# Kernel tuning notes

Measured on AMD Instinct MI355X. Metric: run time of the kernel, lower is better.

The kernel has to match this reference:

```python
import jax, jax.numpy as jnp
import numpy as np

D_MODEL = 1024
NUM_HEADS = 16
NUM_KV_HEADS = 4
D_K = D_MODEL // NUM_HEADS              # 64
G = NUM_HEADS // NUM_KV_HEADS           # queries per kv head = 4
B, S = 2, 2048


def setup_inputs() -> dict:
    key = jax.random.key(0)
    ks = jax.random.split(key, 11)
    s = 0.02
    return {
        "query": jax.random.normal(ks[0], (B, S, D_MODEL), jnp.float32),
        "key_in": jax.random.normal(ks[1], (B, S, D_MODEL), jnp.float32),
        "value_in": jax.random.normal(ks[2], (B, S, D_MODEL), jnp.float32),
        "Wq": jax.random.normal(ks[3], (D_MODEL, D_MODEL), jnp.float32) * s,
        "bq": jnp.zeros((D_MODEL,), jnp.float32),
        "Wk": jax.random.normal(ks[4], (D_MODEL, NUM_KV_HEADS * D_K), jnp.float32) * s,
        "bk": jnp.zeros((NUM_KV_HEADS * D_K,), jnp.float32),
        "Wv": jax.random.normal(ks[5], (D_MODEL, NUM_KV_HEADS * D_K), jnp.float32) * s,
        "bv": jnp.zeros((NUM_KV_HEADS * D_K,), jnp.float32),
        "Wo": jax.random.normal(ks[6], (D_MODEL, D_MODEL), jnp.float32) * s,
        "bo": jnp.zeros((D_MODEL,), jnp.float32),
    }


def reference(query, key_in, value_in, Wq, bq, Wk, bk, Wv, bv, Wo, bo):
    scale = jnp.sqrt(jnp.asarray(D_K, query.dtype))
    # Projections
    Q = (query @ Wq + bq).reshape(B, S, NUM_HEADS, D_K).transpose(0, 2, 1, 3)        # [B,H,S,dk]
    K = (key_in @ Wk + bk).reshape(B, S, NUM_KV_HEADS, D_K).transpose(0, 2, 1, 3)    # [B,KVH,S,dk]
    V = (value_in @ Wv + bv).reshape(B, S, NUM_KV_HEADS, D_K).transpose(0, 2, 1, 3)  # [B,KVH,S,dk]
    # repeat_interleave over head dim -> group Q heads by KV head instead
    Qg = Q.reshape(B, NUM_KV_HEADS, G, S, D_K)                                       # [B,KVH,G,S,dk]
    scores = jnp.einsum('bkgqd,bksd->bkgqs', Qg, K) / scale                          # [B,KVH,G,S,S]
    attn = jax.nn.softmax(scores, axis=-1)
    ctx = jnp.einsum('bkgqs,bksd->bkgqd', attn, V)                                   # [B,KVH,G,S,dk]
    ctx = ctx.reshape(B, NUM_HEADS, S, D_K).transpose(0, 2, 1, 3).reshape(B, S, D_MODEL)
    output = ctx @ Wo + bo
    # new_cache: K[:, ::G] on the repeated tensor == original K/V per kv head
    return output, K, V
```

## Files before the change

kernel.cpp:

```cpp
#include <hip/hip_runtime.h>

typedef unsigned short u16;
typedef unsigned int u32;
typedef __attribute__((ext_vector_type(8))) short short8;
typedef __attribute__((ext_vector_type(4))) float f32x4;

#define MFMA16(a, b, c) __builtin_amdgcn_mfma_f32_16x16x32_bf16(a, b, c, 0, 0, 0)

#define SEQ 2048
#define DM 1024

__device__ __forceinline__ u32 pack2(float a, float b) {
  u32 r;
  asm("v_cvt_pk_bf16_f32 %0, %1, %2" : "=v"(r) : "v"(a), "v"(b));
  return r;
}
__device__ __forceinline__ u32 pack2t(float a, float b) {
  return __builtin_amdgcn_perm(__float_as_uint(b), __float_as_uint(a), 0x07060302u);
}
__device__ __forceinline__ void pswap32(u32& a, u32& b) {
  asm("v_permlane32_swap_b32 %0, %1" : "+v"(a), "+v"(b));
}
__device__ __forceinline__ void pswap16(u32& a, u32& b) {
  asm("v_permlane16_swap_b32 %0, %1" : "+v"(a), "+v"(b));
}
__device__ __forceinline__ void gload16(const u16* g, u16* l) {
  __builtin_amdgcn_global_load_lds((const __attribute__((address_space(1))) u32*)g,
                                   (__attribute__((address_space(3))) u32*)l, 16, 0, 0);
}

#define MBF 0
#define MF32 1
#define MTR 2

template <int AM, int BM>
__device__ __forceinline__ void gemm64(const void* __restrict__ A, const void* __restrict__ B,
                                       int m0, int n0, int ldA, int ldB, u16* lA, u16* lB,
                                       f32x4 acc[2][4]) {
  const int tid = threadIdx.x;
  const int lane = tid & 63, wave = tid >> 6;
  const int l15 = lane & 15, quad = lane >> 4;
  const int wm = wave >> 1, wn = wave & 1;
  const int sr = tid >> 3, sch = tid & 7;
  const int gr = lane >> 3, gch = (lane & 7) ^ (lane >> 3);
  const int nb = tid & 127, ko = tid >> 7;
  f32x4 zero = {0.f, 0.f, 0.f, 0.f};
#pragma unroll
  for (int i = 0; i < 2; i++)
#pragma unroll
    for (int j = 0; j < 4; j++) acc[i][j] = zero;

  float rA[16], rB[32];

  auto issue = [&](int k0, u16* dA, u16* dB) {
    if constexpr (AM == MBF) {
#pragma unroll
      for (int it = 0; it < 2; it++) {
        int w8 = wave * 2 + it;
        gload16((const u16*)A + (size_t)(m0 + w8 * 8 + gr) * ldA + k0 + gch * 8,
                dA + w8 * 512);
      }
    } else if constexpr (AM == MF32) {
#pragma unroll
      for (int it = 0; it < 2; it++) {
        const float* p = (const float*)A + (size_t)(m0 + sr + it * 32) * ldA + k0 + sch * 8;
        float4 a = *(const float4*)p, b = *(const float4*)(p + 4);
        rA[it * 8 + 0] = a.x; rA[it * 8 + 1] = a.y; rA[it * 8 + 2] = a.z; rA[it * 8 + 3] = a.w;
        rA[it * 8 + 4] = b.x; rA[it * 8 + 5] = b.y; rA[it * 8 + 6] = b.z; rA[it * 8 + 7] = b.w;
      }
    } else {
      const float* Wf = (const float*)A;
#pragma unroll
      for (int j = 0; j < 16; j++)
        rA[j] = Wf[(size_t)(k0 + wave * 16 + j) * ldA + m0 + lane];
    }
    if constexpr (BM == MBF) {
#pragma unroll
      for (int it = 0; it < 4; it++) {
        int w8 = wave * 4 + it;
        gload16((const u16*)B + (size_t)(n0 + w8 * 8 + gr) * ldB + k0 + gch * 8,
                dB + w8 * 512);
      }
    } else if constexpr (BM == MF32) {
#pragma unroll
      for (int it = 0; it < 4; it++) {
        const float* p = (const float*)B + (size_t)(n0 + sr + it * 32) * ldB + k0 + sch * 8;
        float4 a = *(const float4*)p, b = *(const float4*)(p + 4);
        rB[it * 8 + 0] = a.x; rB[it * 8 + 1] = a.y; rB[it * 8 + 2] = a.z; rB[it * 8 + 3] = a.w;
        rB[it * 8 + 4] = b.x; rB[it * 8 + 5] = b.y; rB[it * 8 + 6] = b.z; rB[it * 8 + 7] = b.w;
      }
    } else {
      const float* Wf = (const float*)B;
#pragma unroll
      for (int j = 0; j < 32; j++)
        rB[j] = Wf[(size_t)(k0 + ko * 32 + j) * ldB + n0 + nb];
    }
  };

  auto wrb = [&](u16* dA, u16* dB) {
    if constexpr (AM == MF32) {
#pragma unroll
      for (int it = 0; it < 2; it++) {
        int r = sr + it * 32;
        uint4 v;
        v.x = pack2(rA[it * 8 + 0], rA[it * 8 + 1]);
        v.y = pack2(rA[it * 8 + 2], rA[it * 8 + 3]);
        v.z = pack2(rA[it * 8 + 4], rA[it * 8 + 5]);
        v.w = pack2(rA[it * 8 + 6], rA[it * 8 + 7]);
        *(uint4*)&dA[r * 64 + ((sch ^ (r & 7)) << 3)] = v;
      }
    } else if constexpr (AM == MTR) {
#pragma unroll
      for (int o = 0; o < 2; o++) {
        uint4 v;
        v.x = pack2(rA[o * 8 + 0], rA[o * 8 + 1]);
        v.y = pack2(rA[o * 8 + 2], rA[o * 8 + 3]);
        v.z = pack2(rA[o * 8 + 4], rA[o * 8 + 5]);
        v.w = pack2(rA[o * 8 + 6], rA[o * 8 + 7]);
        int c = (wave * 2 + o) ^ (lane & 7);
        *(uint4*)&dA[lane * 64 + (c << 3)] = v;
      }
    }
    if constexpr (BM == MF32) {
#pragma unroll
      for (int it = 0; it < 4; it++) {
        int r = sr + it * 32;
        uint4 v;
        v.x = pack2(rB[it * 8 + 0], rB[it * 8 + 1]);
        v.y = pack2(rB[it * 8 + 2], rB[it * 8 + 3]);
        v.z = pack2(rB[it * 8 + 4], rB[it * 8 + 5]);
        v.w = pack2(rB[it * 8 + 6], rB[it * 8 + 7]);
        *(uint4*)&dB[r * 64 + ((sch ^ (r & 7)) << 3)] = v;
      }
    } else if constexpr (BM == MTR) {
#pragma unroll
      for (int o = 0; o < 4; o++) {
        uint4 v;
        v.x = pack2(rB[o * 8 + 0], rB[o * 8 + 1]);
        v.y = pack2(rB[o * 8 + 2], rB[o * 8 + 3]);
        v.z = pack2(rB[o * 8 + 4], rB[o * 8 + 5]);
        v.w = pack2(rB[o * 8 + 6], rB[o * 8 + 7]);
        int c = (ko * 4 + o) ^ (nb & 7);
        *(uint4*)&dB[nb * 64 + (c << 3)] = v;
      }
    }
  };

  issue(0, lA, lB);
  wrb(lA, lB);
  __syncthreads();

  for (int t = 0; t < 16; t++) {
    u16* cA = lA + (t & 1) * 4096;
    u16* cB = lB + (t & 1) * 8192;
    u16* nA = lA + ((t + 1) & 1) * 4096;
    u16* nB = lB + ((t + 1) & 1) * 8192;
    if (t < 15) issue((t + 1) * 64, nA, nB);
    short8 af[2][2], bfr[4][2];
#pragma unroll
    for (int i = 0; i < 2; i++)
#pragma unroll
      for (int kb = 0; kb < 2; kb++) {
        int r = wm * 32 + i * 16 + l15;
        af[i][kb] = *(const short8*)&cA[r * 64 + (((kb * 4 + quad) ^ (r & 7)) << 3)];
      }
#pragma unroll
    for (int j = 0; j < 4; j++)
#pragma unroll
      for (int kb = 0; kb < 2; kb++) {
        int r = wn * 64 + j * 16 + l15;
        bfr[j][kb] = *(const short8*)&cB[r * 64 + (((kb * 4 + quad) ^ (r & 7)) << 3)];
      }
#pragma unroll
    for (int i = 0; i < 2; i++)
#pragma unroll
      for (int j = 0; j < 4; j++) {
        acc[i][j] = MFMA16(af[i][0], bfr[j][0], acc[i][j]);
        acc[i][j] = MFMA16(af[i][1], bfr[j][1], acc[i][j]);
      }
    if (t < 15) wrb(nA, nB);
    __syncthreads();
  }
}

__global__ __launch_bounds__(256, 3) void k_proj(
    const float* __restrict__ query, const float* __restrict__ key_in,
    const float* __restrict__ value_in, const float* __restrict__ Wq,
    const float* __restrict__ Wk, const float* __restrict__ Wv, const float* __restrict__ bq,
    const float* __restrict__ bk, const float* __restrict__ bv, u16* __restrict__ qbf,
    float* __restrict__ outK, u16* __restrict__ kbf, float* __restrict__ outV,
    u16* __restrict__ vtb, float qscale) {
  __shared__ u16 lA[2 * 4096];
  __shared__ u16 lB[2 * 8192];
  const int idx = blockIdx.x;
  const int lane = threadIdx.x & 63, wave = threadIdx.x >> 6;
  const int l15 = lane & 15, quad = lane >> 4;
  const int wm = wave >> 1, wn = wave & 1;
  f32x4 acc[2][4];

  if (idx < 640) {
    const float* Wt;
    const float* act;
    const float* bias;
    int m0, n0, ldW, mode;
    if (idx < 512) {
      Wt = Wq; act = query; bias = bq; ldW = 1024;
      m0 = (idx >> 5) * 64; n0 = (idx & 31) * 128; mode = 0;
    } else {
      int i2 = idx - 512;
      Wt = Wk; act = key_in; bias = bk; ldW = 256;
      m0 = (i2 >> 5) * 64; n0 = (i2 & 31) * 128; mode = 1;
    }
    gemm64<MTR, MF32>(Wt, act, m0, n0, ldW, 1024, lA, lB, acc);
#pragma unroll
    for (int i = 0; i < 2; i++) {
      int c0 = m0 + wm * 32 + i * 16 + quad * 4;
      float4 bb = *(const float4*)(bias + c0);
#pragma unroll
      for (int j = 0; j < 4; j++) {
        int token = n0 + wn * 64 + j * 16 + l15;
        int b = token >> 11, s = token & 2047;
        float v0 = acc[i][j][0] + bb.x, v1 = acc[i][j][1] + bb.y;
        float v2 = acc[i][j][2] + bb.z, v3 = acc[i][j][3] + bb.w;
        int d = c0 & 63;
        if (mode == 0) {
          int h = c0 >> 6;
          uint2 o;
          o.x = pack2(v0 * qscale, v1 * qscale);
          o.y = pack2(v2 * qscale, v3 * qscale);
          *(uint2*)(qbf + (((size_t)(b * 16 + h) * SEQ + s) << 6) + d) = o;
        } else {
          int kvh = c0 >> 6;
          size_t ix = (((size_t)(b * 4 + kvh) * SEQ + s) << 6) + d;
          float4 vv = {v0, v1, v2, v3};
          *(float4*)(outK + ix) = vv;
          uint2 o;
          o.x = pack2(v0, v1);
          o.y = pack2(v2, v3);
          *(uint2*)(kbf + ix) = o;
        }
      }
    }
  } else {
    int i2 = idx - 640;
    int m0 = (i2 >> 1) * 64, n0 = (i2 & 1) * 128;
    gemm64<MF32, MTR>(value_in, Wv, m0, n0, 1024, 256, lA, lB, acc);
#pragma unroll
    for (int i = 0; i < 2; i++) {
      int r0 = m0 + wm * 32 + i * 16 + quad * 4;
      int b = r0 >> 11, s0 = r0 & 2047;
#pragma unroll
      for (int j = 0; j < 4; j++) {
        int col = n0 + wn * 64 + j * 16 + l15;
        int kvh = col >> 6, d = col & 63;
        float bv_ = bv[col];
        float v0 = acc[i][j][0] + bv_, v1 = acc[i][j][1] + bv_;
        float v2 = acc[i][j][2] + bv_, v3 = acc[i][j][3] + bv_;
        size_t base = (((size_t)(b * 4 + kvh) * SEQ + s0) << 6) + d;
        outV[base] = v0;
        outV[base + 64] = v1;
        outV[base + 128] = v2;
        outV[base + 192] = v3;
        uint2 o;
        o.x = pack2(v0, v1);
        o.y = pack2(v2, v3);
        *(uint2*)(vtb + ((size_t)(b * 4 + kvh) * 64 + d) * SEQ + s0) = o;
      }
    }
  }
}

__global__ __launch_bounds__(256, 2) void k_out(const u16* __restrict__ ctxb,
                                                const float* __restrict__ Wo,
                                                const float* __restrict__ bo,
                                                float* __restrict__ out) {
  __shared__ u16 lA[2 * 4096];
  __shared__ u16 lB[2 * 8192];
  const int idx = blockIdx.x;
  const int m0 = (idx >> 5) * 64, n0 = (idx & 31) * 128;
  const int lane = threadIdx.x & 63, wave = threadIdx.x >> 6;
  const int l15 = lane & 15, quad = lane >> 4;
  const int wm = wave >> 1, wn = wave & 1;
  f32x4 acc[2][4];
  gemm64<MTR, MBF>(Wo, ctxb, m0, n0, 1024, 1024, lA, lB, acc);
#pragma unroll
  for (int i = 0; i < 2; i++) {
    int c0 = m0 + wm * 32 + i * 16 + quad * 4;
    float4 bb = *(const float4*)(bo + c0);
#pragma unroll
    for (int j = 0; j < 4; j++) {
      int token = n0 + wn * 64 + j * 16 + l15;
      float4 vv = {acc[i][j][0] + bb.x, acc[i][j][1] + bb.y, acc[i][j][2] + bb.z,
                   acc[i][j][3] + bb.w};
      *(float4*)(out + (size_t)token * DM + c0) = vv;
    }
  }
}

__global__ __launch_bounds__(256, 2) void k_flash(const u16* __restrict__ Qh,
                                                  const u16* __restrict__ Kb,
                                                  const u16* __restrict__ Vt,
                                                  u16* __restrict__ ctx) {
  __shared__ u16 lK[2][128 * 64];
  __shared__ u16 lV[2][64 * 128];
  const int tid = threadIdx.x;
  const int lane = tid & 63, wave = tid >> 6;
  const int l15 = lane & 15, quad = lane >> 4;
  const int bh = blockIdx.y;
  const int b = bh >> 4, h = bh & 15, kvh = h >> 2;
  const u16* Q = Qh + (size_t)bh * SEQ * 64;
  const u16* Kp = Kb + (size_t)(b * 4 + kvh) * SEQ * 64;
  const u16* Vp = Vt + (size_t)(b * 4 + kvh) * 64 * SEQ;
  const int q0 = blockIdx.x * 128 + wave * 32;

  short8 qf[2][2];
#pragma unroll
  for (int g = 0; g < 2; g++)
#pragma unroll
    for (int kb = 0; kb < 2; kb++)
      qf[g][kb] = *(const short8*)(Q + (size_t)(q0 + g * 16 + l15) * 64 + kb * 32 + quad * 8);

  short8 ones8;
  {
    short ov = (l15 == 0) ? (short)0x3F80 : (short)0;
    ones8 = (short8){ov, ov, ov, ov, ov, ov, ov, ov};
  }

  f32x4 zero = {0.f, 0.f, 0.f, 0.f};
  f32x4 acc[2][4];
  f32x4 lacc[2] = {zero, zero};
#pragma unroll
  for (int g = 0; g < 2; g++)
#pragma unroll
    for (int n = 0; n < 4; n++) acc[g][n] = zero;

  const int gr3 = lane >> 3, gc7 = lane & 7;
  const int gr4 = lane >> 4, gc15 = lane & 15;

  auto stage = [&](int kc, int bufi) {
    u16* dK = lK[bufi];
    u16* dV = lV[bufi];
#pragma unroll
    for (int i = 0; i < 4; i++) {
      int slab = wave * 4 + i;
      gload16(Kp + (size_t)(kc + slab * 8 + gr3) * 64 + ((gc7 ^ gr3) << 3), dK + slab * 512);
    }
#pragma unroll
    for (int i = 0; i < 4; i++) {
      int slab = wave * 4 + i;
      int row = slab * 4 + gr4;
      gload16(Vp + (size_t)row * SEQ + kc + ((gc15 ^ (row & 15)) << 3), dV + slab * 512);
    }
  };

  stage(0, 0);
  __syncthreads();

  for (int t = 0; t < SEQ / 128; t++) {
    if (t < SEQ / 128 - 1) stage((t + 1) * 128, (t + 1) & 1);
    const u16* cK = lK[t & 1];
    const u16* cV = lV[t & 1];

#pragma unroll
    for (int sub = 0; sub < 2; sub++) {
      const int ks = sub * 64;
      f32x4 sc[2][4];
#pragma unroll
      for (int mt = 0; mt < 4; mt++) {
        int row = ks + mt * 16 + l15;
        short8 kf0 = *(const short8*)&cK[row * 64 + ((quad ^ (row & 7)) << 3)];
        short8 kf1 = *(const short8*)&cK[row * 64 + (((4 + quad) ^ (row & 7)) << 3)];
#pragma unroll
        for (int g = 0; g < 2; g++) {
          f32x4 t0 = MFMA16(kf0, qf[g][0], zero);
          sc[g][mt] = MFMA16(kf1, qf[g][1], t0);
        }
      }
#pragma unroll
      for (int g = 0; g < 2; g++)
#pragma unroll
        for (int mt = 0; mt < 4; mt++)
#pragma unroll
          for (int r = 0; r < 4; r++) sc[g][mt][r] = __builtin_amdgcn_exp2f(sc[g][mt][r]);

#pragma unroll
      for (int kbp = 0; kbp < 2; kbp++) {
        short8 pf[2];
#pragma unroll
        for (int g = 0; g < 2; g++) {
          u32 U0 = pack2t(sc[g][2 * kbp][0], sc[g][2 * kbp][1]);
          u32 W0 = pack2t(sc[g][2 * kbp + 1][0], sc[g][2 * kbp + 1][1]);
          u32 U1 = pack2t(sc[g][2 * kbp][2], sc[g][2 * kbp][3]);
          u32 W1 = pack2t(sc[g][2 * kbp + 1][2], sc[g][2 * kbp + 1][3]);
          pswap32(U0, W0);
          pswap16(U0, W0);
          pswap32(U1, W1);
          pswap16(U1, W1);
          u32 w[4] = {U0, U1, W0, W1};
          pf[g] = *(const short8*)w;
        }
        lacc[0] = MFMA16(ones8, pf[0], lacc[0]);
        lacc[1] = MFMA16(ones8, pf[1], lacc[1]);
#pragma unroll
        for (int n = 0; n < 4; n++) {
          int row = n * 16 + l15;
          int chv = sub * 8 + kbp * 4 + quad;
          short8 vf = *(const short8*)&cV[row * 128 + ((chv ^ (row & 15)) << 3)];
          acc[0][n] = MFMA16(vf, pf[0], acc[0][n]);
          acc[1][n] = MFMA16(vf, pf[1], acc[1][n]);
        }
      }
    }
    __syncthreads();
  }

#pragma unroll
  for (int g = 0; g < 2; g++) {
    float lq = __shfl(lacc[g][0], l15);
    float inv = __builtin_amdgcn_rcpf(lq);
    u16* base = ctx + ((size_t)(b * SEQ + q0 + g * 16 + l15)) * DM + h * 64;
#pragma unroll
    for (int n = 0; n < 4; n++) {
      uint2 o;
      o.x = pack2t(acc[g][n][0] * inv, acc[g][n][1] * inv);
      o.y = pack2t(acc[g][n][2] * inv, acc[g][n][3] * inv);
      *(uint2*)(base + n * 16 + quad * 4) = o;
    }
  }
}

extern "C" void kernel_launch(void* const* d_in, const int* in_sizes, int n_in,
                              void* d_out, int out_size, void* d_ws, size_t ws_size,
                              hipStream_t stream) {
  const float* query = (const float*)d_in[0];
  const float* key_in = (const float*)d_in[1];
  const float* value_in = (const float*)d_in[2];
  const float* Wq = (const float*)d_in[3];
  const float* bq = (const float*)d_in[4];
  const float* Wk = (const float*)d_in[5];
  const float* bk = (const float*)d_in[6];
  const float* Wv = (const float*)d_in[7];
  const float* bv = (const float*)d_in[8];
  const float* Wo = (const float*)d_in[9];
  const float* bo = (const float*)d_in[10];

  float* out = (float*)d_out;
  float* outK = out + 4194304;
  float* outV = out + 5242880;

  char* ws = (char*)d_ws;
  u16* qbf = (u16*)(ws + 5242880);
  u16* kbf = (u16*)(ws + 13631488);
  u16* vtb = (u16*)(ws + 15728640);
  u16* ctxb = (u16*)(ws + 17825792);

  const float qscale = 0.125f * 1.44269504088896340736f;

  k_proj<<<dim3(768), 256, 0, stream>>>(query, key_in, value_in, Wq, Wk, Wv, bq, bk, bv,
                                        qbf, outK, kbf, outV, vtb, qscale);
  k_flash<<<dim3(16, 32), 256, 0, stream>>>(qbf, kbf, vtb, ctxb);
  k_out<<<dim3(512), 256, 0, stream>>>(ctxb, Wo, bo, out);
}
```

Measured before the change: 218.0 us.

## Pre-transpose weights and query to bf16 in a prep kernel for async LDS loads

New measurement: 201.3 us. -7.7%, faster.

```diff
diff --git a/kernel.cpp b/kernel.cpp
--- a/kernel.cpp
+++ b/kernel.cpp
@@ -10,6 +10,11 @@
 #define SEQ 2048
 #define DM 1024
 
+__device__ __forceinline__ u16 f2bf(float f) {
+  u32 u = __float_as_uint(f);
+  u += 0x7fffu + ((u >> 16) & 1u);
+  return (u16)(u >> 16);
+}
 __device__ __forceinline__ u32 pack2(float a, float b) {
   u32 r;
   asm("v_cvt_pk_bf16_f32 %0, %1, %2" : "=v"(r) : "v"(a), "v"(b));
@@ -29,9 +34,50 @@
                                    (__attribute__((address_space(3))) u32*)l, 16, 0, 0);
 }
 
+__global__ __launch_bounds__(256) void k_prep(const float* __restrict__ Wq,
+                                              const float* __restrict__ Wk,
+                                              const float* __restrict__ Wv,
+                                              const float* __restrict__ Wo,
+                                              const float* __restrict__ query,
+                                              u16* __restrict__ WqT, u16* __restrict__ WkT,
+                                              u16* __restrict__ WvT, u16* __restrict__ WoT,
+                                              u16* __restrict__ qact) {
+  const int blk = blockIdx.x;
+  const int tid = threadIdx.x;
+  if (blk >= 4096) {
+    size_t base = (size_t)(blk - 4096) * 4096 + tid * 16;
+    const float* p = query + base;
+    uint4 o0, o1;
+    float4 a = *(const float4*)p, b = *(const float4*)(p + 4);
+    float4 c = *(const float4*)(p + 8), d = *(const float4*)(p + 12);
+    o0.x = pack2(a.x, a.y); o0.y = pack2(a.z, a.w);
+    o0.z = pack2(b.x, b.y); o0.w = pack2(b.z, b.w);
+    o1.x = pack2(c.x, c.y); o1.y = pack2(c.z, c.w);
+    o1.z = pack2(d.x, d.y); o1.w = pack2(d.z, d.w);
+    *(uint4*)(qact + base) = o0;
+    *(uint4*)(qact + base + 8) = o1;
+    return;
+  }
+  const int z = blk >> 10, r = blk & 1023;
+  const float* W = z == 0 ? Wq : (z == 1 ? Wk : (z == 2 ? Wv : Wo));
+  u16* Wt = z == 0 ? WqT : (z == 1 ? WkT : (z == 2 ? WvT : WoT));
+  const int N = (z == 1 || z == 2) ? 256 : 1024;
+  const int n0 = (r & 31) * 32;
+  if (n0 >= N) return;
+  const int k0 = (r >> 5) * 32;
+  __shared__ float tile[32][33];
+  int x = tid & 31, y = tid >> 5;
+#pragma unroll
+  for (int i = 0; i < 4; i++)
+    tile[y + i * 8][x] = W[(size_t)(k0 + y + i * 8) * N + n0 + x];
+  __syncthreads();
+#pragma unroll
+  for (int i = 0; i < 4; i++)
+    Wt[(size_t)(n0 + y + i * 8) * 1024 + k0 + x] = f2bf(tile[x][y + i * 8]);
+}
+
 #define MBF 0
 #define MF32 1
-#define MTR 2
 
 template <int AM, int BM>
 __device__ __forceinline__ void gemm64(const void* __restrict__ A, const void* __restrict__ B,
@@ -43,7 +89,6 @@
   const int wm = wave >> 1, wn = wave & 1;
   const int sr = tid >> 3, sch = tid & 7;
   const int gr = lane >> 3, gch = (lane & 7) ^ (lane >> 3);
-  const int nb = tid & 127, ko = tid >> 7;
   f32x4 zero = {0.f, 0.f, 0.f, 0.f};
 #pragma unroll
   for (int i = 0; i < 2; i++)
@@ -60,7 +105,7 @@
         gload16((const u16*)A + (size_t)(m0 + w8 * 8 + gr) * ldA + k0 + gch * 8,
                 dA + w8 * 512);
       }
-    } else if constexpr (AM == MF32) {
+    } else {
 #pragma unroll
       for (int it = 0; it < 2; it++) {
         const float* p = (const float*)A + (size_t)(m0 + sr + it * 32) * ldA + k0 + sch * 8;
@@ -68,11 +113,6 @@
         rA[it * 8 + 0] = a.x; rA[it * 8 + 1] = a.y; rA[it * 8 + 2] = a.z; rA[it * 8 + 3] = a.w;
         rA[it * 8 + 4] = b.x; rA[it * 8 + 5] = b.y; rA[it * 8 + 6] = b.z; rA[it * 8 + 7] = b.w;
       }
-    } else {
-      const float* Wf = (const float*)A;
-#pragma unroll
-      for (int j = 0; j < 16; j++)
-        rA[j] = Wf[(size_t)(k0 + wave * 16 + j) * ldA + m0 + lane];
     }
     if constexpr (BM == MBF) {
 #pragma unroll
@@ -81,7 +121,7 @@
         gload16((const u16*)B + (size_t)(n0 + w8 * 8 + gr) * ldB + k0 + gch * 8,
                 dB + w8 * 512);
       }
-    } else if constexpr (BM == MF32) {
+    } else {
 #pragma unroll
       for (int it = 0; it < 4; it++) {
         const float* p = (const float*)B + (size_t)(n0 + sr + it * 32) * ldB + k0 + sch * 8;
@@ -89,11 +129,6 @@
         rB[it * 8 + 0] = a.x; rB[it * 8 + 1] = a.y; rB[it * 8 + 2] = a.z; rB[it * 8 + 3] = a.w;
         rB[it * 8 + 4] = b.x; rB[it * 8 + 5] = b.y; rB[it * 8 + 6] = b.z; rB[it * 8 + 7] = b.w;
       }
-    } else {
-      const float* Wf = (const float*)B;
-#pragma unroll
-      for (int j = 0; j < 32; j++)
-        rB[j] = Wf[(size_t)(k0 + ko * 32 + j) * ldB + n0 + nb];
     }
   };
 
@@ -109,17 +144,6 @@
         v.w = pack2(rA[it * 8 + 6], rA[it * 8 + 7]);
         *(uint4*)&dA[r * 64 + ((sch ^ (r & 7)) << 3)] = v;
       }
-    } else if constexpr (AM == MTR) {
-#pragma unroll
-      for (int o = 0; o < 2; o++) {
-        uint4 v;
-        v.x = pack2(rA[o * 8 + 0], rA[o * 8 + 1]);
-        v.y = pack2(rA[o * 8 + 2], rA[o * 8 + 3]);
-        v.z = pack2(rA[o * 8 + 4], rA[o * 8 + 5]);
-        v.w = pack2(rA[o * 8 + 6], rA[o * 8 + 7]);
-        int c = (wave * 2 + o) ^ (lane & 7);
-        *(uint4*)&dA[lane * 64 + (c << 3)] = v;
-      }
     }
     if constexpr (BM == MF32) {
 #pragma unroll
@@ -132,17 +156,6 @@
         v.w = pack2(rB[it * 8 + 6], rB[it * 8 + 7]);
         *(uint4*)&dB[r * 64 + ((sch ^ (r & 7)) << 3)] = v;
       }
-    } else if constexpr (BM == MTR) {
-#pragma unroll
-      for (int o = 0; o < 4; o++) {
-        uint4 v;
-        v.x = pack2(rB[o * 8 + 0], rB[o * 8 + 1]);
-        v.y = pack2(rB[o * 8 + 2], rB[o * 8 + 3]);
-        v.z = pack2(rB[o * 8 + 4], rB[o * 8 + 5]);
-        v.w = pack2(rB[o * 8 + 6], rB[o * 8 + 7]);
-        int c = (ko * 4 + o) ^ (nb & 7);
-        *(uint4*)&dB[nb * 64 + (c << 3)] = v;
-      }
     }
   };
 
@@ -184,9 +197,9 @@
 }
 
 __global__ __launch_bounds__(256, 3) void k_proj(
-    const float* __restrict__ query, const float* __restrict__ key_in,
-    const float* __restrict__ value_in, const float* __restrict__ Wq,
-    const float* __restrict__ Wk, const float* __restrict__ Wv, const float* __restrict__ bq,
+    const u16* __restrict__ qact, const float* __restrict__ key_in,
+    const float* __restrict__ value_in, const u16* __restrict__ WqT,
+    const u16* __restrict__ WkT, const u16* __restrict__ WvT, const float* __restrict__ bq,
     const float* __restrict__ bk, const float* __restrict__ bv, u16* __restrict__ qbf,
     float* __restrict__ outK, u16* __restrict__ kbf, float* __restrict__ outV,
     u16* __restrict__ vtb, float qscale) {
@@ -198,53 +211,54 @@
   const int wm = wave >> 1, wn = wave & 1;
   f32x4 acc[2][4];
 
-  if (idx < 640) {
-    const float* Wt;
-    const float* act;
-    const float* bias;
-    int m0, n0, ldW, mode;
-    if (idx < 512) {
-      Wt = Wq; act = query; bias = bq; ldW = 1024;
-      m0 = (idx >> 5) * 64; n0 = (idx & 31) * 128; mode = 0;
-    } else {
-      int i2 = idx - 512;
-      Wt = Wk; act = key_in; bias = bk; ldW = 256;
-      m0 = (i2 >> 5) * 64; n0 = (i2 & 31) * 128; mode = 1;
-    }
-    gemm64<MTR, MF32>(Wt, act, m0, n0, ldW, 1024, lA, lB, acc);
+  if (idx < 512) {
+    int m0 = (idx >> 5) * 64, n0 = (idx & 31) * 128;
+    gemm64<MBF, MBF>(WqT, qact, m0, n0, 1024, 1024, lA, lB, acc);
 #pragma unroll
     for (int i = 0; i < 2; i++) {
       int c0 = m0 + wm * 32 + i * 16 + quad * 4;
-      float4 bb = *(const float4*)(bias + c0);
+      float4 bb = *(const float4*)(bq + c0);
 #pragma unroll
       for (int j = 0; j < 4; j++) {
         int token = n0 + wn * 64 + j * 16 + l15;
         int b = token >> 11, s = token & 2047;
         float v0 = acc[i][j][0] + bb.x, v1 = acc[i][j][1] + bb.y;
         float v2 = acc[i][j][2] + bb.z, v3 = acc[i][j][3] + bb.w;
-        int d = c0 & 63;
-        if (mode == 0) {
-          int h = c0 >> 6;
-          uint2 o;
-          o.x = pack2(v0 * qscale, v1 * qscale);
-          o.y = pack2(v2 * qscale, v3 * qscale);
-          *(uint2*)(qbf + (((size_t)(b * 16 + h) * SEQ + s) << 6) + d) = o;
-        } else {
-          int kvh = c0 >> 6;
-          size_t ix = (((size_t)(b * 4 + kvh) * SEQ + s) << 6) + d;
-          float4 vv = {v0, v1, v2, v3};
-          *(float4*)(outK + ix) = vv;
-          uint2 o;
-          o.x = pack2(v0, v1);
-          o.y = pack2(v2, v3);
-          *(uint2*)(kbf + ix) = o;
-        }
+        int d = c0 & 63, h = c0 >> 6;
+        uint2 o;
+        o.x = pack2(v0 * qscale, v1 * qscale);
+        o.y = pack2(v2 * qscale, v3 * qscale);
+        *(uint2*)(qbf + (((size_t)(b * 16 + h) * SEQ + s) << 6) + d) = o;
+      }
+    }
+  } else if (idx < 640) {
+    int i2 = idx - 512;
+    int m0 = (i2 >> 5) * 64, n0 = (i2 & 31) * 128;
+    gemm64<MBF, MF32>(WkT, key_in, m0, n0, 1024, 1024, lA, lB, acc);
+#pragma unroll
+    for (int i = 0; i < 2; i++) {
+      int c0 = m0 + wm * 32 + i * 16 + quad * 4;
+      float4 bb = *(const float4*)(bk + c0);
+#pragma unroll
+      for (int j = 0; j < 4; j++) {
+        int token = n0 + wn * 64 + j * 16 + l15;
+        int b = token >> 11, s = token & 2047;
+        float v0 = acc[i][j][0] + bb.x, v1 = acc[i][j][1] + bb.y;
+        float v2 = acc[i][j][2] + bb.z, v3 = acc[i][j][3] + bb.w;
+        int d = c0 & 63, kvh = c0 >> 6;
+        size_t ix = (((size_t)(b * 4 + kvh) * SEQ + s) << 6) + d;
+        float4 vv = {v0, v1, v2, v3};
+        *(float4*)(outK + ix) = vv;
+        uint2 o;
+        o.x = pack2(v0, v1);
+        o.y = pack2(v2, v3);
+        *(uint2*)(kbf + ix) = o;
       }
     }
   } else {
     int i2 = idx - 640;
     int m0 = (i2 >> 1) * 64, n0 = (i2 & 1) * 128;
-    gemm64<MF32, MTR>(value_in, Wv, m0, n0, 1024, 256, lA, lB, acc);
+    gemm64<MF32, MBF>(value_in, WvT, m0, n0, 1024, 1024, lA, lB, acc);
 #pragma unroll
     for (int i = 0; i < 2; i++) {
       int r0 = m0 + wm * 32 + i * 16 + quad * 4;
@@ -270,8 +284,8 @@
   }
 }
 
-__global__ __launch_bounds__(256, 2) void k_out(const u16* __restrict__ ctxb,
-                                                const float* __restrict__ Wo,
+__global__ __launch_bounds__(256, 3) void k_out(const u16* __restrict__ ctxb,
+                                                const u16* __restrict__ WoT,
                                                 const float* __restrict__ bo,
                                                 float* __restrict__ out) {
   __shared__ u16 lA[2 * 4096];
@@ -282,7 +296,7 @@
   const int l15 = lane & 15, quad = lane >> 4;
   const int wm = wave >> 1, wn = wave & 1;
   f32x4 acc[2][4];
-  gemm64<MTR, MBF>(Wo, ctxb, m0, n0, 1024, 1024, lA, lB, acc);
+  gemm64<MBF, MBF>(WoT, ctxb, m0, n0, 1024, 1024, lA, lB, acc);
 #pragma unroll
   for (int i = 0; i < 2; i++) {
     int c0 = m0 + wm * 32 + i * 16 + quad * 4;
@@ -449,15 +463,21 @@
   float* outV = out + 5242880;
 
   char* ws = (char*)d_ws;
-  u16* qbf = (u16*)(ws + 5242880);
-  u16* kbf = (u16*)(ws + 13631488);
-  u16* vtb = (u16*)(ws + 15728640);
-  u16* ctxb = (u16*)(ws + 17825792);
+  u16* WqT = (u16*)(ws);
+  u16* WkT = (u16*)(ws + 2097152);
+  u16* WvT = (u16*)(ws + 2621440);
+  u16* WoT = (u16*)(ws + 3145728);
+  u16* qact = (u16*)(ws + 5242880);
+  u16* ctxb = (u16*)(ws + 5242880);
+  u16* qbf = (u16*)(ws + 13631488);
+  u16* kbf = (u16*)(ws + 22020096);
+  u16* vtb = (u16*)(ws + 24117248);
 
   const float qscale = 0.125f * 1.44269504088896340736f;
 
-  k_proj<<<dim3(768), 256, 0, stream>>>(query, key_in, value_in, Wq, Wk, Wv, bq, bk, bv,
+  k_prep<<<dim3(5120), 256, 0, stream>>>(Wq, Wk, Wv, Wo, query, WqT, WkT, WvT, WoT, qact);
+  k_proj<<<dim3(768), 256, 0, stream>>>(qact, key_in, value_in, WqT, WkT, WvT, bq, bk, bv,
                                         qbf, outK, kbf, outV, vtb, qscale);
   k_flash<<<dim3(16, 32), 256, 0, stream>>>(qbf, kbf, vtb, ctxb);
-  k_out<<<dim3(512), 256, 0, stream>>>(ctxb, Wo, bo, out);
-}
+  k_out<<<dim3(512), 256, 0, stream>>>(ctxb, WoT, bo, out);
+}
```

## Fuse Q projection into flash kernel and pre-convert weights to bf16

Applied to the files above, without the earlier changes.

Measured after the change: 208.1 us. 4.6% less time.

```diff
diff --git a/kernel.cpp b/kernel.cpp
--- a/kernel.cpp
+++ b/kernel.cpp
@@ -10,6 +10,11 @@
 #define SEQ 2048
 #define DM 1024
 
+__device__ __forceinline__ u16 f2bf(float f) {
+  u32 u = __float_as_uint(f);
+  u += 0x7fffu + ((u >> 16) & 1u);
+  return (u16)(u >> 16);
+}
 __device__ __forceinline__ u32 pack2(float a, float b) {
   u32 r;
   asm("v_cvt_pk_bf16_f32 %0, %1, %2" : "=v"(r) : "v"(a), "v"(b));
@@ -183,124 +188,110 @@
   }
 }
 
-__global__ __launch_bounds__(256, 3) void k_proj(
-    const float* __restrict__ query, const float* __restrict__ key_in,
-    const float* __restrict__ value_in, const float* __restrict__ Wq,
-    const float* __restrict__ Wk, const float* __restrict__ Wv, const float* __restrict__ bq,
-    const float* __restrict__ bk, const float* __restrict__ bv, u16* __restrict__ qbf,
-    float* __restrict__ outK, u16* __restrict__ kbf, float* __restrict__ outV,
-    u16* __restrict__ vtb, float qscale) {
-  __shared__ u16 lA[2 * 4096];
-  __shared__ u16 lB[2 * 8192];
+__global__ __launch_bounds__(256, 3) void k_pre(
+    const float* __restrict__ Wq, const float* __restrict__ Wk, const float* __restrict__ Wv,
+    const float* __restrict__ Wo, const float* __restrict__ query,
+    const float* __restrict__ key_in, const float* __restrict__ value_in,
+    const float* __restrict__ bk, const float* __restrict__ bv, u16* __restrict__ WqT,
+    u16* __restrict__ WoT, u16* __restrict__ qact, float* __restrict__ outK,
+    u16* __restrict__ kbf, float* __restrict__ outV, u16* __restrict__ vtb) {
+  __shared__ u16 lsd[2 * 4096 + 2 * 8192];
   const int idx = blockIdx.x;
-  const int lane = threadIdx.x & 63, wave = threadIdx.x >> 6;
-  const int l15 = lane & 15, quad = lane >> 4;
-  const int wm = wave >> 1, wn = wave & 1;
-  f32x4 acc[2][4];
-
-  if (idx < 640) {
-    const float* Wt;
-    const float* act;
-    const float* bias;
-    int m0, n0, ldW, mode;
-    if (idx < 512) {
-      Wt = Wq; act = query; bias = bq; ldW = 1024;
-      m0 = (idx >> 5) * 64; n0 = (idx & 31) * 128; mode = 0;
-    } else {
-      int i2 = idx - 512;
-      Wt = Wk; act = key_in; bias = bk; ldW = 256;
-      m0 = (i2 >> 5) * 64; n0 = (i2 & 31) * 128; mode = 1;
-    }
-    gemm64<MTR, MF32>(Wt, act, m0, n0, ldW, 1024, lA, lB, acc);
-#pragma unroll
-    for (int i = 0; i < 2; i++) {
-      int c0 = m0 + wm * 32 + i * 16 + quad * 4;
-      float4 bb = *(const float4*)(bias + c0);
-#pragma unroll
-      for (int j = 0; j < 4; j++) {
-        int token = n0 + wn * 64 + j * 16 + l15;
-        int b = token >> 11, s = token & 2047;
-        float v0 = acc[i][j][0] + bb.x, v1 = acc[i][j][1] + bb.y;
-        float v2 = acc[i][j][2] + bb.z, v3 = acc[i][j][3] + bb.w;
-        int d = c0 & 63;
-        if (mode == 0) {
-          int h = c0 >> 6;
-          uint2 o;
-          o.x = pack2(v0 * qscale, v1 * qscale);
-          o.y = pack2(v2 * qscale, v3 * qscale);
-          *(uint2*)(qbf + (((size_t)(b * 16 + h) * SEQ + s) << 6) + d) = o;
-        } else {
-          int kvh = c0 >> 6;
+  const int tid = threadIdx.x;
+
+  if (idx < 256) {
+    u16* lA = lsd;
+    u16* lB = lsd + 2 * 4096;
+    const int lane = tid & 63, wave = tid >> 6;
+    const int l15 = lane & 15, quad = lane >> 4;
+    const int wm = wave >> 1, wn = wave & 1;
+    f32x4 acc[2][4];
+    if (idx < 128) {
+      int m0 = (idx >> 5) * 64, n0 = (idx & 31) * 128;
+      gemm64<MTR, MF32>(Wk, key_in, m0, n0, 256, 1024, lA, lB, acc);
+#pragma unroll
+      for (int i = 0; i < 2; i++) {
+        int c0 = m0 + wm * 32 + i * 16 + quad * 4;
+        float4 bb = *(const float4*)(bk + c0);
+#pragma unroll
+        for (int j = 0; j < 4; j++) {
+          int token = n0 + wn * 64 + j * 16 + l15;
+          int b = token >> 11, s = token & 2047;
+          float v0 = acc[i][j][0] + bb.x, v1 = acc[i][j][1] + bb.y;
+          float v2 = acc[i][j][2] + bb.z, v3 = acc[i][j][3] + bb.w;
+          int d = c0 & 63, kvh = c0 >> 6;
           size_t ix = (((size_t)(b * 4 + kvh) * SEQ + s) << 6) + d;
           float4 vv = {v0, v1, v2, v3};
           *(float4*)(outK + ix) = vv;
-          uint2 o;
-          o.x = pack2(v0, v1);
-          o.y = pack2(v2, v3);
-          *(uint2*)(kbf + ix) = o;
+          uint2 ob;
+          ob.x = pack2(v0, v1);
+          ob.y = pack2(v2, v3);
+          *(uint2*)(kbf + ix) = ob;
         }
       }
-    }
+    } else {
+      int vi = idx - 128;
+      int m0 = (vi >> 1) * 64, n0 = (vi & 1) * 128;
+      gemm64<MF32, MTR>(value_in, Wv, m0, n0, 1024, 256, lA, lB, acc);
+#pragma unroll
+      for (int i = 0; i < 2; i++) {
+        int r0 = m0 + wm * 32 + i * 16 + quad * 4;
+        int b = r0 >> 11, s0 = r0 & 2047;
+#pragma unroll
+        for (int j = 0; j < 4; j++) {
+          int col = n0 + wn * 64 + j * 16 + l15;
+          int kvh = col >> 6, d = col & 63;
+          float bv_ = bv[col];
+          float v0 = acc[i][j][0] + bv_, v1 = acc[i][j][1] + bv_;
+          float v2 = acc[i][j][2] + bv_, v3 = acc[i][j][3] + bv_;
+          size_t base = (((size_t)(b * 4 + kvh) * SEQ + s0) << 6) + d;
+          outV[base] = v0;
+          outV[base + 64] = v1;
+          outV[base + 128] = v2;
+          outV[base + 192] = v3;
+          uint2 ob;
+          ob.x = pack2(v0, v1);
+          ob.y = pack2(v2, v3);
+          *(uint2*)(vtb + ((size_t)(b * 4 + kvh) * 64 + d) * SEQ + s0) = ob;
+        }
+      }
+    }
+  } else if (idx < 2304) {
+    float(*tile)[33] = (float(*)[33])lsd;
+    int wi = idx - 256;
+    const float* W = wi < 1024 ? Wq : Wo;
+    u16* Wt = wi < 1024 ? WqT : WoT;
+    wi &= 1023;
+    const int n0 = (wi & 31) * 32, k0 = (wi >> 5) * 32;
+    int x = tid & 31, y = tid >> 5;
+#pragma unroll
+    for (int i = 0; i < 4; i++)
+      tile[y + i * 8][x] = W[(size_t)(k0 + y + i * 8) * 1024 + n0 + x];
+    __syncthreads();
+#pragma unroll
+    for (int i = 0; i < 4; i++)
+      Wt[(size_t)(n0 + y + i * 8) * 1024 + k0 + x] = f2bf(tile[x][y + i * 8]);
   } else {
-    int i2 = idx - 640;
-    int m0 = (i2 >> 1) * 64, n0 = (i2 & 1) * 128;
-    gemm64<MF32, MTR>(value_in, Wv, m0, n0, 1024, 256, lA, lB, acc);
-#pragma unroll
-    for (int i = 0; i < 2; i++) {
-      int r0 = m0 + wm * 32 + i * 16 + quad * 4;
-      int b = r0 >> 11, s0 = r0 & 2047;
-#pragma unroll
-      for (int j = 0; j < 4; j++) {
-        int col = n0 + wn * 64 + j * 16 + l15;
-        int kvh = col >> 6, d = col & 63;
-        float bv_ = bv[col];
-        float v0 = acc[i][j][0] + bv_, v1 = acc[i][j][1] + bv_;
-        float v2 = acc[i][j][2] + bv_, v3 = acc[i][j][3] + bv_;
-        size_t base = (((size_t)(b * 4 + kvh) * SEQ + s0) << 6) + d;
-        outV[base] = v0;
-        outV[base + 64] = v1;
-        outV[base + 128] = v2;
-        outV[base + 192] = v3;
-        uint2 o;
-        o.x = pack2(v0, v1);
-        o.y = pack2(v2, v3);
-        *(uint2*)(vtb + ((size_t)(b * 4 + kvh) * 64 + d) * SEQ + s0) = o;
-      }
-    }
-  }
-}
-
-__global__ __launch_bounds__(256, 2) void k_out(const u16* __restrict__ ctxb,
-                                                const float* __restrict__ Wo,
-                                                const float* __restrict__ bo,
-                                                float* __restrict__ out) {
-  __shared__ u16 lA[2 * 4096];
-  __shared__ u16 lB[2 * 8192];
-  const int idx = blockIdx.x;
-  const int m0 = (idx >> 5) * 64, n0 = (idx & 31) * 128;
-  const int lane = threadIdx.x & 63, wave = threadIdx.x >> 6;
-  const int l15 = lane & 15, quad = lane >> 4;
-  const int wm = wave >> 1, wn = wave & 1;
-  f32x4 acc[2][4];
-  gemm64<MTR, MBF>(Wo, ctxb, m0, n0, 1024, 1024, lA, lB, acc);
-#pragma unroll
-  for (int i = 0; i < 2; i++) {
-    int c0 = m0 + wm * 32 + i * 16 + quad * 4;
-    float4 bb = *(const float4*)(bo + c0);
-#pragma unroll
-    for (int j = 0; j < 4; j++) {
-      int token = n0 + wn * 64 + j * 16 + l15;
-      float4 vv = {acc[i][j][0] + bb.x, acc[i][j][1] + bb.y, acc[i][j][2] + bb.z,
-                   acc[i][j][3] + bb.w};
-      *(float4*)(out + (size_t)token * DM + c0) = vv;
-    }
-  }
-}
-
-__global__ __launch_bounds__(256, 2) void k_flash(const u16* __restrict__ Qh,
+    size_t base = (size_t)(idx - 2304) * 4096 + tid * 16;
+    const float* p = query + base;
+    uint4 o0, o1;
+    float4 a = *(const float4*)p, b = *(const float4*)(p + 4);
+    float4 c = *(const float4*)(p + 8), d = *(const float4*)(p + 12);
+    o0.x = pack2(a.x, a.y); o0.y = pack2(a.z, a.w);
+    o0.z = pack2(b.x, b.y); o0.w = pack2(b.z, b.w);
+    o1.x = pack2(c.x, c.y); o1.y = pack2(c.z, c.w);
+    o1.z = pack2(d.x, d.y); o1.w = pack2(d.z, d.w);
+    *(uint4*)(qact + base) = o0;
+    *(uint4*)(qact + base + 8) = o1;
+  }
+}
+
+__global__ __launch_bounds__(256, 2) void k_flash(const u16* __restrict__ qact,
+                                                  const u16* __restrict__ WqT,
+                                                  const float* __restrict__ bq,
                                                   const u16* __restrict__ Kb,
                                                   const u16* __restrict__ Vt,
-                                                  u16* __restrict__ ctx) {
+                                                  u16* __restrict__ ctx, float qscale) {
   __shared__ u16 lK[2][128 * 64];
   __shared__ u16 lV[2][64 * 128];
   const int tid = threadIdx.x;
@@ -308,17 +299,41 @@
   const int l15 = lane & 15, quad = lane >> 4;
   const int bh = blockIdx.y;
   const int b = bh >> 4, h = bh & 15, kvh = h >> 2;
-  const u16* Q = Qh + (size_t)bh * SEQ * 64;
   const u16* Kp = Kb + (size_t)(b * 4 + kvh) * SEQ * 64;
   const u16* Vp = Vt + (size_t)(b * 4 + kvh) * 64 * SEQ;
-  const int q0 = blockIdx.x * 128 + wave * 32;
+  const int wm = wave >> 1, wn = wave & 1;
+
+  u16* lA = (u16*)lK;
+  u16* lB = (u16*)lV;
+  u16* lQ = (u16*)lK + 8192;
+  {
+    f32x4 qa[2][4];
+    gemm64<MBF, MBF>(WqT, qact, h * 64, b * SEQ + blockIdx.x * 128, 1024, 1024, lA, lB, qa);
+#pragma unroll
+    for (int i = 0; i < 2; i++) {
+      int c0 = wm * 32 + i * 16 + quad * 4;
+      float4 bb = *(const float4*)(bq + h * 64 + c0);
+#pragma unroll
+      for (int j = 0; j < 4; j++) {
+        int row = wn * 64 + j * 16 + l15;
+        uint2 o;
+        o.x = pack2((qa[i][j][0] + bb.x) * qscale, (qa[i][j][1] + bb.y) * qscale);
+        o.y = pack2((qa[i][j][2] + bb.z) * qscale, (qa[i][j][3] + bb.w) * qscale);
+        int chq = c0 >> 3;
+        *(uint2*)&lQ[row * 64 + ((chq ^ (row & 7)) << 3) + (quad & 1) * 4] = o;
+      }
+    }
+  }
+  __syncthreads();
 
   short8 qf[2][2];
 #pragma unroll
   for (int g = 0; g < 2; g++)
 #pragma unroll
-    for (int kb = 0; kb < 2; kb++)
-      qf[g][kb] = *(const short8*)(Q + (size_t)(q0 + g * 16 + l15) * 64 + kb * 32 + quad * 8);
+    for (int kb = 0; kb < 2; kb++) {
+      int row = wave * 32 + g * 16 + l15;
+      qf[g][kb] = *(const short8*)&lQ[row * 64 + (((kb * 4 + quad) ^ (row & 7)) << 3)];
+    }
 
   short8 ones8;
   {
@@ -336,6 +351,7 @@
 
   const int gr3 = lane >> 3, gc7 = lane & 7;
   const int gr4 = lane >> 4, gc15 = lane & 15;
+  const int q0 = blockIdx.x * 128 + wave * 32;
 
   auto stage = [&](int kc, int bufi) {
     u16* dK = lK[bufi];
@@ -353,6 +369,7 @@
     }
   };
 
+  __syncthreads();
   stage(0, 0);
   __syncthreads();
 
@@ -429,6 +446,33 @@
   }
 }
 
+__global__ __launch_bounds__(256, 3) void k_out(const u16* __restrict__ ctxb,
+                                                const u16* __restrict__ WoT,
+                                                const float* __restrict__ bo,
+                                                float* __restrict__ out) {
+  __shared__ u16 lA[2 * 4096];
+  __shared__ u16 lB[2 * 8192];
+  const int idx = blockIdx.x;
+  const int m0 = (idx >> 5) * 64, n0 = (idx & 31) * 128;
+  const int lane = threadIdx.x & 63, wave = threadIdx.x >> 6;
+  const int l15 = lane & 15, quad = lane >> 4;
+  const int wm = wave >> 1, wn = wave & 1;
+  f32x4 acc[2][4];
+  gemm64<MBF, MBF>(WoT, ctxb, m0, n0, 1024, 1024, lA, lB, acc);
+#pragma unroll
+  for (int i = 0; i < 2; i++) {
+    int c0 = m0 + wm * 32 + i * 16 + quad * 4;
+    float4 bb = *(const float4*)(bo + c0);
+#pragma unroll
+    for (int j = 0; j < 4; j++) {
+      int token = n0 + wn * 64 + j * 16 + l15;
+      float4 vv = {acc[i][j][0] + bb.x, acc[i][j][1] + bb.y, acc[i][j][2] + bb.z,
+                   acc[i][j][3] + bb.w};
+      *(float4*)(out + (size_t)token * DM + c0) = vv;
+    }
+  }
+}
+
 extern "C" void kernel_launch(void* const* d_in, const int* in_sizes, int n_in,
                               void* d_out, int out_size, void* d_ws, size_t ws_size,
                               hipStream_t stream) {
@@ -449,15 +493,17 @@
   float* outV = out + 5242880;
 
   char* ws = (char*)d_ws;
-  u16* qbf = (u16*)(ws + 5242880);
-  u16* kbf = (u16*)(ws + 13631488);
-  u16* vtb = (u16*)(ws + 15728640);
-  u16* ctxb = (u16*)(ws + 17825792);
+  u16* WqT = (u16*)(ws);
+  u16* WoT = (u16*)(ws + 2097152);
+  u16* qact = (u16*)(ws + 4194304);
+  u16* ctxb = (u16*)(ws + 12582912);
+  u16* kbf = (u16*)(ws + 20971520);
+  u16* vtb = (u16*)(ws + 23068672);
 
   const float qscale = 0.125f * 1.44269504088896340736f;
 
-  k_proj<<<dim3(768), 256, 0, stream>>>(query, key_in, value_in, Wq, Wk, Wv, bq, bk, bv,
-                                        qbf, outK, kbf, outV, vtb, qscale);
-  k_flash<<<dim3(16, 32), 256, 0, stream>>>(qbf, kbf, vtb, ctxb);
-  k_out<<<dim3(512), 256, 0, stream>>>(ctxb, Wo, bo, out);
-}
+  k_pre<<<dim3(3328), 256, 0, stream>>>(Wq, Wk, Wv, Wo, query, key_in, value_in, bk, bv,
+                                        WqT, WoT, qact, outK, kbf, outV, vtb);
+  k_flash<<<dim3(16, 32), 256, 0, stream>>>(qact, WqT, bq, kbf, vtb, ctxb, qscale);
+  k_out<<<dim3(512), 256, 0, stream>>>(ctxb, WoT, bo, out);
+}
```
